# Kernel optimization log

Measured on AMD Instinct MI355X. Metric: run time of the kernel, lower is better.

## Reference

```python
import jax, jax.numpy as jnp
import numpy as np
import math

B, S, H, HKV, DH = 2, 2048, 32, 1, 128  # batch, seq, q heads, kv heads, per-head/model dim
D_K = 128


def setup_inputs() -> dict:
    key = jax.random.key(0)
    ks = jax.random.split(key, 11)
    sc = 0.02
    return {
        "query": jax.random.normal(ks[0], (B, S, DH), jnp.float32),
        "key": jax.random.normal(ks[1], (B, S, DH), jnp.float32),
        "values": jax.random.normal(ks[2], (B, S, DH), jnp.float32),
        "W_q": jax.random.normal(ks[3], (DH, H * DH), jnp.float32) * sc,
        "b_q": jnp.zeros((H * DH,), jnp.float32),
        "W_k": jax.random.normal(ks[4], (DH, HKV * DH), jnp.float32) * sc,
        "b_k": jnp.zeros((HKV * DH,), jnp.float32),
        "W_v": jax.random.normal(ks[5], (DH, HKV * DH), jnp.float32) * sc,
        "b_v": jnp.zeros((HKV * DH,), jnp.float32),
        "W_o": jax.random.normal(ks[6], (H * DH, DH), jnp.float32) * sc,
        "b_o": jnp.zeros((DH,), jnp.float32),
    }


def reference(query, key, values, W_q, b_q, W_k, b_k, W_v, b_v, W_o, b_o):
    # Projections (note: the original uses raw .view(-1, H, S, DH), which we
    # replicate exactly — it is a reshape, not a transpose).
    q = (query @ W_q + b_q).reshape(-1, H, S, DH)      # [B,H,S,DH]
    k = (key @ W_k + b_k).reshape(-1, HKV, S, DH)       # [B,1,S,DH]
    v = (values @ W_v + b_v).reshape(-1, HKV, S, DH)    # [B,1,S,DH]

    # RoPE outputs in the original forward are computed but never used
    # (dead code), and mask defaults to None -> no masking. Dropout omitted
    # for deterministic reference.
    scores = jnp.matmul(q, jnp.swapaxes(k, -1, -2)) / math.sqrt(D_K)  # [B,H,S,S]
    attn = jax.nn.softmax(scores, axis=-1)
    out = jnp.matmul(attn, v)                           # [B,H,S,DH]
    out = jnp.swapaxes(out, 1, 2).reshape(-1, S, H * DH)
    return out @ W_o + b_o                              # [B,S,DH]
```

## Files before the change

### kernel.cpp

```cpp
#include <hip/hip_runtime.h>
#include <hip/hip_bf16.h>
#include <math.h>


typedef __hip_bfloat16 bf16;
typedef __attribute__((ext_vector_type(8))) short short8;
typedef __attribute__((ext_vector_type(4))) float floatx4;

static constexpr int B_ = 2;
static constexpr int S_ = 2048;
static constexpr int H_ = 32;
static constexpr int DH_ = 128;

#define GL16(gp, lp)                                              \
  __builtin_amdgcn_global_load_lds(                               \
      (const __attribute__((address_space(1))) void*)(gp),        \
      (__attribute__((address_space(3))) void*)(lp), 16, 0, 0)

__global__ void detect_dtype(const unsigned short* __restrict__ q,
                             int* __restrict__ flag) {
  int t = threadIdx.x;
  int cnt = 0;
#pragma unroll
  for (int i = 0; i < 8; ++i) {
    unsigned short u = q[t * 8 + i];
    int e = (u >> 7) & 0xFF;
    if (e < 0x60) cnt++;
  }
#pragma unroll
  for (int off = 1; off < 64; off <<= 1) cnt += __shfl_xor(cnt, off);
  if (t == 0) *flag = (cnt >= 8) ? 1 : 0;
}

__global__ void cvt3_bf16(const void* __restrict__ a, const void* __restrict__ b,
                          const void* __restrict__ c, bf16* __restrict__ da,
                          bf16* __restrict__ db, bf16* __restrict__ dc, int n,
                          const int* __restrict__ flag) {
  int i = blockIdx.x * 256 + threadIdx.x;
  if (i >= n) return;
  const void* s = (blockIdx.y == 0) ? a : (blockIdx.y == 1) ? b : c;
  bf16* d = (blockIdx.y == 0) ? da : (blockIdx.y == 1) ? db : dc;
  d[i] = (*flag) ? __float2bfloat16(((const float*)s)[i]) : ((const bf16*)s)[i];
}

__global__ void cvt_biases(const void* __restrict__ bq, const void* __restrict__ bk,
                           const void* __restrict__ bv, const void* __restrict__ bo,
                           float* __restrict__ fq, float* __restrict__ fk,
                           float* __restrict__ fv, float* __restrict__ fo,
                           const int* __restrict__ flag, float qscale) {
  int i = blockIdx.x * 256 + threadIdx.x;
  const void* s;
  float* d;
  int off;
  float sc = 1.f;
  if (i < 4096) { s = bq; d = fq; off = i; sc = qscale; }
  else if (i < 4224) { s = bk; d = fk; off = i - 4096; }
  else if (i < 4352) { s = bv; d = fv; off = i - 4224; }
  else if (i < 4480) { s = bo; d = fo; off = i - 4352; }
  else return;
  float v = (*flag) ? ((const float*)s)[off]
                    : __bfloat162float(((const bf16*)s)[off]);
  d[off] = v * sc;
}

__global__ void ttranspose(const void* __restrict__ W, bf16* __restrict__ Wt,
                           int K, int N, const int* __restrict__ flag,
                           float scale) {
  __shared__ bf16 tile[64][66];
  int n0 = blockIdx.x * 64, k0 = blockIdx.y * 64;
  int c = threadIdx.x & 63;
  int r4 = threadIdx.x >> 6;
  bool f = (*flag) != 0;
#pragma unroll
  for (int i = 0; i < 16; ++i) {
    int r = r4 * 16 + i;
    float v = f ? ((const float*)W)[(size_t)(k0 + r) * N + n0 + c]
                : __bfloat162float(((const bf16*)W)[(size_t)(k0 + r) * N + n0 + c]);
    tile[r][c] = __float2bfloat16(v * scale);
  }
  __syncthreads();
#pragma unroll
  for (int i = 0; i < 16; ++i) {
    int cc = r4 * 16 + i;
    Wt[(size_t)(n0 + cc) * K + k0 + c] = tile[c][cc];
  }
}

__global__ void init_out32(float* __restrict__ out32,
                           const float* __restrict__ bias, int n) {
  int i = blockIdx.x * 256 + threadIdx.x;
  if (i < n) out32[i] = bias[i & 127];
}

template <int MODE>
__global__ __launch_bounds__(256) void gemm2(
    const bf16* __restrict__ A, int lda, const bf16* __restrict__ Bt, int ldb,
    const float* __restrict__ bias, bf16* __restrict__ Cb,
    float* __restrict__ Cf, int K_len, int ldc) {
  const int lane = threadIdx.x & 63;
  const int wave = threadIdx.x >> 6;
  const int lm = lane & 15;
  const int quad = lane >> 4;
  const int row_base = blockIdx.y * 64 + wave * 16;
  const int col_base = blockIdx.x * 64;
  const int koff = blockIdx.z * K_len;

  const bf16* arow = A + (size_t)(row_base + lm) * lda + koff + quad * 8;
  const bf16* brow = Bt + (size_t)(col_base + lm) * ldb + koff + quad * 8;

  floatx4 z = {0.f, 0.f, 0.f, 0.f};
  floatx4 acc[4] = {z, z, z, z};

  for (int kk = 0; kk < K_len; kk += 32) {
    short8 a = *(const short8*)(arow + kk);
#pragma unroll
    for (int t = 0; t < 4; ++t) {
      short8 b = *(const short8*)(brow + (size_t)(t * 16) * ldb + kk);
      acc[t] = __builtin_amdgcn_mfma_f32_16x16x32_bf16(a, b, acc[t], 0, 0, 0);
    }
  }

#pragma unroll
  for (int t = 0; t < 4; ++t) {
    int col = col_base + t * 16 + lm;
#pragma unroll
    for (int r = 0; r < 4; ++r) {
      int row = row_base + quad * 4 + r;
      if (MODE == 0) {
        Cb[(size_t)row * ldc + col] = __float2bfloat16(acc[t][r] + bias[col]);
      } else if (MODE == 3) {
        Cb[((size_t)((row >> 11) * DH_ + col)) * S_ + (row & 2047)] =
            __float2bfloat16(acc[t][r] + bias[col]);
      } else {
        atomicAdd(&Cf[(size_t)row * ldc + col], acc[t][r]);
      }
    }
  }
}

static __device__ __forceinline__ unsigned bpack(float lo, float hi) {
  union { bf16 h; unsigned short u; } a, b;
  a.h = __float2bfloat16(lo);
  b.h = __float2bfloat16(hi);
  return (unsigned)a.u | ((unsigned)b.u << 16);
}

static __device__ __forceinline__ void pexchange(const unsigned pk[8],
                                                 int quad, short8* pf) {
  const bool q0 = (quad & 1);
  unsigned sA0 = q0 ? pk[0] : pk[2];
  unsigned sA1 = q0 ? pk[1] : pk[3];
  unsigned sA2 = q0 ? pk[4] : pk[6];
  unsigned sA3 = q0 ? pk[5] : pk[7];
  unsigned r0 = (unsigned)__shfl_xor((int)sA0, 16);
  unsigned r1 = (unsigned)__shfl_xor((int)sA1, 16);
  unsigned r2 = (unsigned)__shfl_xor((int)sA2, 16);
  unsigned r3 = (unsigned)__shfl_xor((int)sA3, 16);
  unsigned M0 = q0 ? r0 : pk[0];
  unsigned M1 = q0 ? r1 : pk[1];
  unsigned M2 = q0 ? pk[2] : r0;
  unsigned M3 = q0 ? pk[3] : r1;
  unsigned M4 = q0 ? r2 : pk[4];
  unsigned M5 = q0 ? r3 : pk[5];
  unsigned M6 = q0 ? pk[6] : r2;
  unsigned M7 = q0 ? pk[7] : r3;
  const bool swp = (quad == 1) || (quad == 2);
  union { unsigned u[4]; short8 v; } f0, f1;
  unsigned t0, t1;
  t0 = (unsigned)__shfl_xor((int)M0, 48); f0.u[0] = swp ? t0 : M0;
  t1 = (unsigned)__shfl_xor((int)M1, 48); f0.u[1] = swp ? t1 : M1;
  t0 = (unsigned)__shfl_xor((int)M2, 48); f0.u[2] = swp ? t0 : M2;
  t1 = (unsigned)__shfl_xor((int)M3, 48); f0.u[3] = swp ? t1 : M3;
  t0 = (unsigned)__shfl_xor((int)M4, 48); f1.u[0] = swp ? t0 : M4;
  t1 = (unsigned)__shfl_xor((int)M5, 48); f1.u[1] = swp ? t1 : M5;
  t0 = (unsigned)__shfl_xor((int)M6, 48); f1.u[2] = swp ? t0 : M6;
  t1 = (unsigned)__shfl_xor((int)M7, 48); f1.u[3] = swp ? t1 : M7;
  pf[0] = f0.v;
  pf[1] = f1.v;
}

__global__ __launch_bounds__(256, 2) void flash_attn(
    const bf16* __restrict__ Qp, const bf16* __restrict__ Kp,
    const bf16* __restrict__ Vt, bf16* __restrict__ O2c) {
  const int tid = threadIdx.x;
  const int lane = tid & 63;
  const int wave = tid >> 6;
  const int lm = lane & 15;
  const int quad = lane >> 4;
  const int qt = blockIdx.x;
  const int h = blockIdx.y;
  const int b = blockIdx.z;

  __shared__ __align__(16) bf16 Klds[2][64 * 128];
  __shared__ __align__(16) bf16 Vlds[2][128 * 64];

  const int base = qt * 128 + wave * 32;
  const bf16* qrow = Qp + ((size_t)b * S_ + h * 64 + (base >> 5)) * 4096;
  short8 qf0[4], qf1[4];
#pragma unroll
  for (int ks = 0; ks < 4; ++ks) {
    qf0[ks] = *(const short8*)(qrow + lm * 128 + quad * 8 + ks * 32);
    qf1[ks] = *(const short8*)(qrow + (16 + lm) * 128 + quad * 8 + ks * 32);
  }

  const bf16* Kb = Kp + (size_t)b * S_ * DH_;
  const bf16* Vb = Vt + (size_t)b * DH_ * S_;
  const int sw = lm & 7;

  const bf16* kgp[4];
  const bf16* vgp[4];
#pragma unroll
  for (int i = 0; i < 4; ++i) {
    const int inst = wave * 4 + i;
    const int krow = inst * 4 + quad;
    kgp[i] = Kb + (size_t)krow * 128 + ((lm ^ (krow & 7)) * 8);
    const int vrow = inst * 8 + (lane >> 3);
    vgp[i] = Vb + (size_t)vrow * S_ + (((lane & 7) ^ (vrow & 7)) * 8);
  }

  floatx4 z = {0.f, 0.f, 0.f, 0.f};
  floatx4 oa0[8], oa1[8];
#pragma unroll
  for (int nt = 0; nt < 8; ++nt) { oa0[nt] = z; oa1[nt] = z; }
  float ls0 = 0.f, ls1 = 0.f;

#pragma unroll
  for (int i = 0; i < 4; ++i) {
    GL16(kgp[i], &Klds[0][(wave * 4 + i) * 512]);
    GL16(vgp[i], &Vlds[0][(wave * 4 + i) * 512]);
    kgp[i] += 64 * 128;
    vgp[i] += 64;
  }
  __syncthreads();

  int cur = 0;
  for (int kb = 0; kb < S_; kb += 64) {
    const bf16* Kc = Klds[cur];
    const bf16* Vc = Vlds[cur];
    if (kb + 64 < S_) {
      bf16* Kn = Klds[cur ^ 1];
      bf16* Vn = Vlds[cur ^ 1];
#pragma unroll
      for (int i = 0; i < 4; ++i) {
        GL16(kgp[i], Kn + (wave * 4 + i) * 512);
        GL16(vgp[i], Vn + (wave * 4 + i) * 512);
        kgp[i] += 64 * 128;
        vgp[i] += 64;
      }
    }

    floatx4 s0[4] = {z, z, z, z}, s1[4] = {z, z, z, z};
    __builtin_amdgcn_s_setprio(1);
#pragma unroll
    for (int t = 0; t < 4; ++t) {
#pragma unroll
      for (int ks = 0; ks < 4; ++ks) {
        short8 kf = *(const short8*)(&Kc[(t * 16 + lm) * 128 +
                                         (((quad + 4 * ks) ^ sw) * 8)]);
        s0[t] = __builtin_amdgcn_mfma_f32_16x16x32_bf16(kf, qf0[ks], s0[t],
                                                        0, 0, 0);
        s1[t] = __builtin_amdgcn_mfma_f32_16x16x32_bf16(kf, qf1[ks], s1[t],
                                                        0, 0, 0);
      }
    }
    __builtin_amdgcn_s_setprio(0);

    unsigned pk0[8], pk1[8];
#pragma unroll
    for (int t = 0; t < 4; ++t) {
      float a0 = __expf(s0[t][0]), a1 = __expf(s0[t][1]);
      float a2 = __expf(s0[t][2]), a3 = __expf(s0[t][3]);
      ls0 += (a0 + a1) + (a2 + a3);
      pk0[2 * t] = bpack(a0, a1);
      pk0[2 * t + 1] = bpack(a2, a3);
      float c0 = __expf(s1[t][0]), c1 = __expf(s1[t][1]);
      float c2 = __expf(s1[t][2]), c3 = __expf(s1[t][3]);
      ls1 += (c0 + c1) + (c2 + c3);
      pk1[2 * t] = bpack(c0, c1);
      pk1[2 * t + 1] = bpack(c2, c3);
    }
    short8 pf0[2], pf1[2];
    pexchange(pk0, quad, pf0);
    pexchange(pk1, quad, pf1);

    __builtin_amdgcn_s_setprio(1);
#pragma unroll
    for (int ks2 = 0; ks2 < 2; ++ks2) {
#pragma unroll
      for (int nt = 0; nt < 8; ++nt) {
        short8 vf = *(const short8*)(&Vc[(nt * 16 + lm) * 64 +
                                         (((quad + 4 * ks2) ^ sw) * 8)]);
        oa0[nt] = __builtin_amdgcn_mfma_f32_16x16x32_bf16(pf0[ks2], vf,
                                                          oa0[nt], 0, 0, 0);
        oa1[nt] = __builtin_amdgcn_mfma_f32_16x16x32_bf16(pf1[ks2], vf,
                                                          oa1[nt], 0, 0, 0);
      }
    }
    __builtin_amdgcn_s_setprio(0);
    __syncthreads();
    cur ^= 1;
  }

  ls0 += __shfl_xor(ls0, 16);
  ls0 += __shfl_xor(ls0, 32);
  ls1 += __shfl_xor(ls1, 16);
  ls1 += __shfl_xor(ls1, 32);
  float inv0[4], inv1[4];
#pragma unroll
  for (int r = 0; r < 4; ++r) {
    inv0[r] = 1.0f / __shfl(ls0, quad * 4 + r);
    inv1[r] = 1.0f / __shfl(ls1, quad * 4 + r);
  }

#pragma unroll
  for (int r = 0; r < 4; ++r) {
    int s2a = base + quad * 4 + r;
    int s2b = s2a + 16;
    size_t ba = ((size_t)b * S_ + s2a) * 4096 + (size_t)h * 128;
    size_t bb = ((size_t)b * S_ + s2b) * 4096 + (size_t)h * 128;
#pragma unroll
    for (int nt = 0; nt < 8; ++nt) {
      O2c[ba + nt * 16 + lm] = __float2bfloat16(oa0[nt][r] * inv0[r]);
      O2c[bb + nt * 16 + lm] = __float2bfloat16(oa1[nt][r] * inv1[r]);
    }
  }
}

extern "C" void kernel_launch(void* const* d_in, const int* in_sizes, int n_in,
                              void* d_out, int out_size, void* d_ws,
                              size_t ws_size, hipStream_t stream) {
  (void)in_sizes;
  (void)n_in;
  (void)out_size;
  (void)ws_size;

  const void* query = d_in[0];
  const void* key = d_in[1];
  const void* values = d_in[2];
  const void* W_q = d_in[3];
  const void* b_q = d_in[4];
  const void* W_k = d_in[5];
  const void* b_k = d_in[6];
  const void* W_v = d_in[7];
  const void* b_v = d_in[8];
  const void* W_o = d_in[9];
  const void* b_o = d_in[10];
  float* out = (float*)d_out;

  const float kScale = 0.08838834764831845f;
  const int M = B_ * S_;
  const int QN = B_ * S_ * DH_;
  const int ON = QN;

  char* w = (char*)d_ws;
  auto carve = [&](size_t bytes) -> char* {
    char* p = w;
    w += (bytes + 255) & ~(size_t)255;
    return p;
  };
  int* flag = (int*)carve(4);
  bf16* cQ = (bf16*)carve((size_t)QN * 2);
  bf16* cK = (bf16*)carve((size_t)QN * 2);
  bf16* cV = (bf16*)carve((size_t)QN * 2);
  float* fbq = (float*)carve((size_t)H_ * DH_ * 4);
  float* fbk = (float*)carve((size_t)DH_ * 4);
  float* fbv = (float*)carve((size_t)DH_ * 4);
  float* fbo = (float*)carve((size_t)DH_ * 4);
  bf16* Wqt = (bf16*)carve((size_t)DH_ * H_ * DH_ * 2);
  bf16* Wkt = (bf16*)carve((size_t)DH_ * DH_ * 2);
  bf16* Wvt = (bf16*)carve((size_t)DH_ * DH_ * 2);
  bf16* Wot = (bf16*)carve((size_t)H_ * DH_ * DH_ * 2);
  bf16* Kp = (bf16*)carve((size_t)B_ * S_ * DH_ * 2);
  bf16* Vtp = (bf16*)carve((size_t)B_ * S_ * DH_ * 2);
  bf16* Qp = (bf16*)carve((size_t)M * H_ * DH_ * 2);
  bf16* O2c = (bf16*)carve((size_t)M * H_ * DH_ * 2);

  detect_dtype<<<1, 64, 0, stream>>>((const unsigned short*)query, flag);
  cvt3_bf16<<<dim3(QN / 256, 3), 256, 0, stream>>>(query, key, values, cQ, cK,
                                                   cV, QN, flag);
  cvt_biases<<<18, 256, 0, stream>>>(b_q, b_k, b_v, b_o, fbq, fbk, fbv, fbo,
                                     flag, kScale);

  ttranspose<<<dim3(H_ * DH_ / 64, DH_ / 64), 256, 0, stream>>>(
      W_q, Wqt, DH_, H_ * DH_, flag, kScale);
  ttranspose<<<dim3(DH_ / 64, DH_ / 64), 256, 0, stream>>>(W_k, Wkt, DH_, DH_,
                                                           flag, 1.0f);
  ttranspose<<<dim3(DH_ / 64, DH_ / 64), 256, 0, stream>>>(W_v, Wvt, DH_, DH_,
                                                           flag, 1.0f);
  ttranspose<<<dim3(DH_ / 64, H_ * DH_ / 64), 256, 0, stream>>>(
      W_o, Wot, H_ * DH_, DH_, flag, 1.0f);

  gemm2<0><<<dim3(2, 64), 256, 0, stream>>>(cK, DH_, Wkt, DH_, fbk, Kp,
                                            nullptr, DH_, DH_);
  gemm2<3><<<dim3(2, 64), 256, 0, stream>>>(cV, DH_, Wvt, DH_, fbv, Vtp,
                                            nullptr, DH_, 0);
  gemm2<0><<<dim3(64, 64), 256, 0, stream>>>(cQ, DH_, Wqt, DH_, fbq, Qp,
                                             nullptr, DH_, H_ * DH_);

  init_out32<<<ON / 256, 256, 0, stream>>>(out, fbo, ON);

  flash_attn<<<dim3(S_ / 128, H_, B_), 256, 0, stream>>>(Qp, Kp, Vtp, O2c);

  gemm2<4><<<dim3(DH_ / 64, M / 64, 8), 256, 0, stream>>>(
      O2c, H_ * DH_, Wot, H_ * DH_, nullptr, nullptr, out,
      (H_ * DH_) / 8, DH_);
}
```

Baseline: 375.5 us.

## Replace split-K atomics with partial buffers plus reduce kernel; use exp2 softmax

The output projection stops accumulating its 8 K-splits into the output with float atomics. It now uses 4 K-splits, each writing plain stores into a partial buffer that reuses the dead Qp workspace, and a new finish_out kernel sums the four partials and adds the bias with float4 loads. This drops the separate bias-init kernel and removes atomic contention. Separately, the query scale now folds in log2(e) so the softmax can call exp2f instead of __expf, saving a multiply per exponent. The extra reduce kernel adds about 8 MB of memory traffic and one more launch.

```diff
diff --git a/kernel.cpp b/kernel.cpp
--- a/kernel.cpp
+++ b/kernel.cpp
@@ -86,12 +86,6 @@
   }
 }
 
-__global__ void init_out32(float* __restrict__ out32,
-                           const float* __restrict__ bias, int n) {
-  int i = blockIdx.x * 256 + threadIdx.x;
-  if (i < n) out32[i] = bias[i & 127];
-}
-
 template <int MODE>
 __global__ __launch_bounds__(256) void gemm2(
     const bf16* __restrict__ A, int lda, const bf16* __restrict__ Bt, int ldb,
@@ -132,10 +126,29 @@
         Cb[((size_t)((row >> 11) * DH_ + col)) * S_ + (row & 2047)] =
             __float2bfloat16(acc[t][r] + bias[col]);
       } else {
-        atomicAdd(&Cf[(size_t)row * ldc + col], acc[t][r]);
+        Cf[(size_t)blockIdx.z * (4096 * 128) + (size_t)row * ldc + col] =
+            acc[t][r];
       }
     }
   }
+}
+
+__global__ void finish_out(const float* __restrict__ parts,
+                           const float* __restrict__ bias,
+                           float* __restrict__ out) {
+  int i = blockIdx.x * 256 + threadIdx.x;
+  const float4* p = (const float4*)parts;
+  float4 a = p[i];
+  float4 b = p[i + 131072];
+  float4 c = p[i + 262144];
+  float4 d = p[i + 393216];
+  float4 bb = ((const float4*)bias)[i & 31];
+  float4 o;
+  o.x = a.x + b.x + c.x + d.x + bb.x;
+  o.y = a.y + b.y + c.y + d.y + bb.y;
+  o.z = a.z + b.z + c.z + d.z + bb.z;
+  o.w = a.w + b.w + c.w + d.w + bb.w;
+  ((float4*)out)[i] = o;
 }
 
 static __device__ __forceinline__ unsigned bpack(float lo, float hi) {
@@ -144,6 +157,8 @@
   b.h = __float2bfloat16(hi);
   return (unsigned)a.u | ((unsigned)b.u << 16);
 }
+
+static __device__ __forceinline__ float fexp2(float x) { return exp2f(x); }
 
 static __device__ __forceinline__ void pexchange(const unsigned pk[8],
                                                  int quad, short8* pf) {
@@ -268,13 +283,13 @@
     unsigned pk0[8], pk1[8];
 #pragma unroll
     for (int t = 0; t < 4; ++t) {
-      float a0 = __expf(s0[t][0]), a1 = __expf(s0[t][1]);
-      float a2 = __expf(s0[t][2]), a3 = __expf(s0[t][3]);
+      float a0 = fexp2(s0[t][0]), a1 = fexp2(s0[t][1]);
+      float a2 = fexp2(s0[t][2]), a3 = fexp2(s0[t][3]);
       ls0 += (a0 + a1) + (a2 + a3);
       pk0[2 * t] = bpack(a0, a1);
       pk0[2 * t + 1] = bpack(a2, a3);
-      float c0 = __expf(s1[t][0]), c1 = __expf(s1[t][1]);
-      float c2 = __expf(s1[t][2]), c3 = __expf(s1[t][3]);
+      float c0 = fexp2(s1[t][0]), c1 = fexp2(s1[t][1]);
+      float c2 = fexp2(s1[t][2]), c3 = fexp2(s1[t][3]);
       ls1 += (c0 + c1) + (c2 + c3);
       pk1[2 * t] = bpack(c0, c1);
       pk1[2 * t + 1] = bpack(c2, c3);
@@ -347,10 +362,9 @@
   const void* b_o = d_in[10];
   float* out = (float*)d_out;
 
-  const float kScale = 0.08838834764831845f;
+  const float kScale = 0.1275174388204085f;
   const int M = B_ * S_;
   const int QN = B_ * S_ * DH_;
-  const int ON = QN;
 
   char* w = (char*)d_ws;
   auto carve = [&](size_t bytes) -> char* {
@@ -375,6 +389,8 @@
   bf16* Qp = (bf16*)carve((size_t)M * H_ * DH_ * 2);
   bf16* O2c = (bf16*)carve((size_t)M * H_ * DH_ * 2);
 
+  float* parts = (float*)Qp;
+
   detect_dtype<<<1, 64, 0, stream>>>((const unsigned short*)query, flag);
   cvt3_bf16<<<dim3(QN / 256, 3), 256, 0, stream>>>(query, key, values, cQ, cK,
                                                    cV, QN, flag);
@@ -397,11 +413,11 @@
   gemm2<0><<<dim3(64, 64), 256, 0, stream>>>(cQ, DH_, Wqt, DH_, fbq, Qp,
                                              nullptr, DH_, H_ * DH_);
 
-  init_out32<<<ON / 256, 256, 0, stream>>>(out, fbo, ON);
-
   flash_attn<<<dim3(S_ / 128, H_, B_), 256, 0, stream>>>(Qp, Kp, Vtp, O2c);
 
-  gemm2<4><<<dim3(DH_ / 64, M / 64, 8), 256, 0, stream>>>(
-      O2c, H_ * DH_, Wot, H_ * DH_, nullptr, nullptr, out,
-      (H_ * DH_) / 8, DH_);
-}
+  gemm2<4><<<dim3(DH_ / 64, M / 64, 4), 256, 0, stream>>>(
+      O2c, H_ * DH_, Wot, H_ * DH_, nullptr, nullptr, parts,
+      (H_ * DH_) / 4, DH_);
+
+  finish_out<<<QN / 4 / 256, 256, 0, stream>>>(parts, fbo, out);
+}
```

Result: slower. 400.0 us (+6.5%).
